# Kernel tuning notes

Hardware: AMD Instinct MI355X
Metric: run time of the kernel (lower is better)

## Reference

```python
import jax, jax.numpy as jnp
import numpy as np
import math

B, S, D, H = 2, 2048, 1024, 16
DK = D // H


def setup_inputs() -> dict:
    key = jax.random.key(0)
    ks = jax.random.split(key, 11)
    s = 1.0 / math.sqrt(D)
    return {
        "q": jax.random.normal(ks[0], (B, S, D), jnp.float32),
        "k": jax.random.normal(ks[1], (B, S, D), jnp.float32),
        "v": jax.random.normal(ks[2], (B, S, D), jnp.float32),
        "Wq": jax.random.normal(ks[3], (D, D), jnp.float32) * s,
        "bq": jnp.zeros((D,), jnp.float32),
        "Wk": jax.random.normal(ks[4], (D, D), jnp.float32) * s,
        "bk": jnp.zeros((D,), jnp.float32),
        "Wv": jax.random.normal(ks[5], (D, D), jnp.float32) * s,
        "bv": jnp.zeros((D,), jnp.float32),
        "Wo": jax.random.normal(ks[6], (D, D), jnp.float32) * s,
        "bo": jnp.zeros((D,), jnp.float32),
        "mask": jnp.ones((B, 1, S), dtype=bool),
    }


def reference(q, k, v, Wq, bq, Wk, bk, Wv, bv, Wo, bo, mask):
    # project and split heads: [B,S,D] -> [B,H,S,DK]
    def proj(x, W, b):
        return (x @ W.T + b).reshape(B, S, H, DK).transpose(0, 2, 1, 3)

    qh, kh, vh = proj(q, Wq, bq), proj(k, Wk, bk), proj(v, Wv, bv)
    scores = jnp.einsum("bhqd,bhkd->bhqk", qh, kh) / math.sqrt(DK)
    # 3D mask [B,1,S], self-attn: expand to [B,1,S,S] via outer AND
    m = mask[:, :, None, :] & mask[:, :, :, None]
    scores = jnp.where(m, scores, -1e9)
    attn = jax.nn.softmax(scores, axis=-1)
    attn = jnp.nan_to_num(attn, nan=0.0, posinf=0.0, neginf=0.0)
    out = jnp.einsum("bhqk,bhkd->bhqd", attn, vh)  # [B,H,S,DK]
    concat = out.transpose(0, 2, 1, 3).reshape(B, S, D)
    return concat @ Wo.T + bo
```

## Files before the change

kernel.cpp:

```cpp
#include <hip/hip_runtime.h>
#include <hip/hip_bf16.h>
#include <stdint.h>

using bf16 = __bf16;
typedef __attribute__((ext_vector_type(8))) __bf16 bf16x8;
typedef __attribute__((ext_vector_type(4))) float f32x4;

typedef const __attribute__((address_space(1))) void* gptr_t;
typedef __attribute__((address_space(3))) void* lptr_t;

__device__ __forceinline__ void gld16(const void* g, void* l) {
    __builtin_amdgcn_global_load_lds((gptr_t)g, (lptr_t)l, 16, 0, 0);
}

__global__ __launch_bounds__(256)
void cvt_kern(const float* __restrict__ in, bf16* __restrict__ out, int n)
{
    const int i = (blockIdx.x * 256 + threadIdx.x) * 8;
    if (i >= n) return;
    const float4 f0 = *(const float4*)(in + i);
    const float4 f1 = *(const float4*)(in + i + 4);
    bf16x8 v = { (bf16)f0.x, (bf16)f0.y, (bf16)f0.z, (bf16)f0.w,
                 (bf16)f1.x, (bf16)f1.y, (bf16)f1.z, (bf16)f1.w };
    *(bf16x8*)(out + i) = v;
}

template<int MODE, bool XWS, bool OUTF32>
__global__ __launch_bounds__(256, 2)
void gemm_mfma(const void* __restrict__ Xv, const bf16* __restrict__ W,
               const float* __restrict__ bias, void* __restrict__ Yv)
{
    constexpr int K = 1024, N = 1024;
    __shared__ bf16 As[64 * 64];
    __shared__ bf16 Bs[128 * 64];

    const int t = threadIdx.x;
    const int w = t >> 6, lane = t & 63, quad = lane >> 4, l15 = lane & 15;
    const int m0 = blockIdx.y * 64, n0 = blockIdx.x * 128;
    const int wm = (w >> 1) * 32, wn = (w & 1) * 64;

    const int srow = t >> 3;
    const int sseg = (t & 7) ^ (srow & 7);

    const float* Xf = (const float*)Xv;
    const bf16*  gA16 = (const bf16*)Xv + (size_t)(m0 + srow) * K + sseg * 8;
    const bf16*  gB   = W + (size_t)(n0 + srow) * K + sseg * 8;

    f32x4 acc[2][4] = {};

    for (int k0 = 0; k0 < K; k0 += 64) {
        if (XWS) {
            gld16(gA16 + k0,          As + t * 8);
            gld16(gA16 + k0 + 32 * K, As + t * 8 + 2048);
        } else {
            #pragma unroll
            for (int r = 0; r < 2; ++r) {
                const int g = r * 256 + t;
                const int row = g >> 3, sg = g & 7;
                const float* p = Xf + (size_t)(m0 + row) * K + k0 + sg * 8;
                const float4 f0 = *(const float4*)p;
                const float4 f1 = *(const float4*)(p + 4);
                bf16x8 vv = { (bf16)f0.x, (bf16)f0.y, (bf16)f0.z, (bf16)f0.w,
                              (bf16)f1.x, (bf16)f1.y, (bf16)f1.z, (bf16)f1.w };
                *(bf16x8*)&As[row * 64 + ((sg ^ (row & 7)) * 8)] = vv;
            }
        }
        gld16(gB + k0,            Bs + t * 8);
        gld16(gB + k0 + 32 * K,   Bs + t * 8 + 2048);
        gld16(gB + k0 + 64 * K,   Bs + t * 8 + 4096);
        gld16(gB + k0 + 96 * K,   Bs + t * 8 + 6144);
        __syncthreads();

        bf16x8 af[2][2], bfr[4][2];
        #pragma unroll
        for (int mt = 0; mt < 2; ++mt)
            #pragma unroll
            for (int kt = 0; kt < 2; ++kt) {
                const int row = wm + mt * 16 + l15;
                const int seg = (kt * 4 + quad) ^ (row & 7);
                af[mt][kt] = *(const bf16x8*)&As[row * 64 + seg * 8];
            }
        #pragma unroll
        for (int nt = 0; nt < 4; ++nt)
            #pragma unroll
            for (int kt = 0; kt < 2; ++kt) {
                const int row = wn + nt * 16 + l15;
                const int seg = (kt * 4 + quad) ^ (row & 7);
                bfr[nt][kt] = *(const bf16x8*)&Bs[row * 64 + seg * 8];
            }
        #pragma unroll
        for (int kt = 0; kt < 2; ++kt)
            #pragma unroll
            for (int mt = 0; mt < 2; ++mt)
                #pragma unroll
                for (int nt = 0; nt < 4; ++nt)
                    acc[mt][nt] = __builtin_amdgcn_mfma_f32_16x16x32_bf16(
                        af[mt][kt], bfr[nt][kt], acc[mt][nt], 0, 0, 0);
        __syncthreads();
    }

    #pragma unroll
    for (int nt = 0; nt < 4; ++nt) {
        const int col = n0 + wn + nt * 16 + l15;
        const float bv = bias[col];
        #pragma unroll
        for (int mt = 0; mt < 2; ++mt)
            #pragma unroll
            for (int i = 0; i < 4; ++i) {
                const int row = m0 + wm + mt * 16 + quad * 4 + i;
                const float v = acc[mt][nt][i] + bv;
                if (MODE == 0) {
                    const size_t off = (size_t)row * N + col;
                    if (OUTF32) ((float*)Yv)[off] = v;
                    else        ((bf16*)Yv)[off]  = (bf16)v;
                } else {
                    const int b = row >> 11, s = row & 2047;
                    const int h = col >> 6, d = col & 63;
                    ((bf16*)Yv)[(((size_t)(b * 16 + h) * 64 + d) << 11) + s] = (bf16)v;
                }
            }
    }
}

__global__ __launch_bounds__(256, 2)
void attn_mfma(const bf16* __restrict__ Q, const bf16* __restrict__ Kg,
               const bf16* __restrict__ Vt, bf16* Cc)
{
    constexpr int S = 2048, D = 1024, DK = 64, LDP = 72;
    __shared__ bf16 Qs[128 * 64];
    __shared__ bf16 Ks[64 * 64];
    __shared__ bf16 Vs[80 * 64];
    __shared__ bf16 Ps[4][32 * LDP];

    const int t = threadIdx.x;
    const int w = t >> 6, lane = t & 63, quad = lane >> 4, l15 = lane & 15;
    const int bh = blockIdx.y, b = bh >> 4, h = bh & 15;
    const int q0 = blockIdx.x * 128;
    const int wq = w * 32;

    const int srow = t >> 3;
    const int sseg = (t & 7) ^ (srow & 7);

    for (int i = t; i < 16 * 64; i += 256) {
        const int r = 64 + (i >> 6);
        Vs[r * 64 + (i & 63)] = (r == 64) ? (bf16)1.0f : (bf16)0.0f;
    }

    {
        const bf16* gQ = Q + (size_t)(b * S + q0 + srow) * D + h * DK + sseg * 8;
        #pragma unroll
        for (int r = 0; r < 4; ++r)
            gld16(gQ + (size_t)(r * 32) * D, Qs + t * 8 + r * 2048);
    }
    __syncthreads();

    bf16x8 aq[2][2];
    #pragma unroll
    for (int mt = 0; mt < 2; ++mt)
        #pragma unroll
        for (int kt = 0; kt < 2; ++kt) {
            const int row = wq + mt * 16 + l15;
            const int seg = (kt * 4 + quad) ^ (row & 7);
            aq[mt][kt] = *(const bf16x8*)&Qs[row * 64 + seg * 8];
        }

    f32x4 o[2][5] = {};
    float mrow[2][4];
    #pragma unroll
    for (int mt = 0; mt < 2; ++mt)
        #pragma unroll
        for (int i = 0; i < 4; ++i) mrow[mt][i] = -1e30f;

    const float c = 0.125f * 1.44269504088896340736f;

    const bf16* gK = Kg + (size_t)(b * S + srow) * D + h * DK + sseg * 8;
    const bf16* gV = Vt + ((size_t)bh * DK + srow) * S + sseg * 8;

    for (int s0 = 0; s0 < S; s0 += 64) {
        gld16(gK + (size_t)s0 * D,        Ks + t * 8);
        gld16(gK + (size_t)(s0 + 32) * D, Ks + t * 8 + 2048);
        gld16(gV + s0,                    Vs + t * 8);
        gld16(gV + s0 + 32 * S,           Vs + t * 8 + 2048);
        __syncthreads();

        f32x4 sa[2][4] = {};
        bf16x8 bk[4][2];
        #pragma unroll
        for (int nt = 0; nt < 4; ++nt)
            #pragma unroll
            for (int kt = 0; kt < 2; ++kt) {
                const int row = nt * 16 + l15;
                const int seg = (kt * 4 + quad) ^ (row & 7);
                bk[nt][kt] = *(const bf16x8*)&Ks[row * 64 + seg * 8];
            }
        #pragma unroll
        for (int kt = 0; kt < 2; ++kt)
            #pragma unroll
            for (int mt = 0; mt < 2; ++mt)
                #pragma unroll
                for (int nt = 0; nt < 4; ++nt)
                    sa[mt][nt] = __builtin_amdgcn_mfma_f32_16x16x32_bf16(
                        aq[mt][kt], bk[nt][kt], sa[mt][nt], 0, 0, 0);

        #pragma unroll
        for (int mt = 0; mt < 2; ++mt)
            #pragma unroll
            for (int i = 0; i < 4; ++i) {
                float v = fmaxf(fmaxf(sa[mt][0][i], sa[mt][1][i]),
                                fmaxf(sa[mt][2][i], sa[mt][3][i])) * c;
                v = fmaxf(v, __shfl_xor(v, 1));
                v = fmaxf(v, __shfl_xor(v, 2));
                v = fmaxf(v, __shfl_xor(v, 4));
                v = fmaxf(v, __shfl_xor(v, 8));
                const float mnew = fmaxf(mrow[mt][i], v);
                const float alpha = __builtin_amdgcn_exp2f(mrow[mt][i] - mnew);
                mrow[mt][i] = mnew;

                const int prow = mt * 16 + quad * 4 + i;
                #pragma unroll
                for (int nt = 0; nt < 4; ++nt) {
                    const float pv = __builtin_amdgcn_exp2f(sa[mt][nt][i] * c - mnew);
                    Ps[w][prow * LDP + nt * 16 + l15] = (bf16)pv;
                }
                #pragma unroll
                for (int nt = 0; nt < 5; ++nt)
                    o[mt][nt][i] *= alpha;
            }

        bf16x8 ap[2][2], bvv[5][2];
        #pragma unroll
        for (int mt = 0; mt < 2; ++mt)
            #pragma unroll
            for (int kt = 0; kt < 2; ++kt) {
                const int row = mt * 16 + l15;
                ap[mt][kt] = *(const bf16x8*)&Ps[w][row * LDP + kt * 32 + quad * 8];
            }
        #pragma unroll
        for (int nt = 0; nt < 5; ++nt)
            #pragma unroll
            for (int kt = 0; kt < 2; ++kt) {
                const int row = nt * 16 + l15;
                const int seg = (kt * 4 + quad) ^ (row & 7);
                bvv[nt][kt] = *(const bf16x8*)&Vs[row * 64 + seg * 8];
            }
        #pragma unroll
        for (int kt = 0; kt < 2; ++kt)
            #pragma unroll
            for (int mt = 0; mt < 2; ++mt)
                #pragma unroll
                for (int nt = 0; nt < 5; ++nt)
                    o[mt][nt] = __builtin_amdgcn_mfma_f32_16x16x32_bf16(
                        ap[mt][kt], bvv[nt][kt], o[mt][nt], 0, 0, 0);

        __syncthreads();
    }

    #pragma unroll
    for (int mt = 0; mt < 2; ++mt)
        #pragma unroll
        for (int i = 0; i < 4; ++i) {
            const int row = q0 + wq + mt * 16 + quad * 4 + i;
            const float lsum = __shfl(o[mt][4][i], quad << 4);
            const float inv = 1.0f / lsum;
            #pragma unroll
            for (int nt = 0; nt < 4; ++nt) {
                const int col = nt * 16 + l15;
                Cc[(size_t)(b * S + row) * D + h * DK + col] = (bf16)(o[mt][nt][i] * inv);
            }
        }
}

extern "C" void kernel_launch(void* const* d_in, const int* in_sizes, int n_in,
                              void* d_out, int out_size, void* d_ws, size_t ws_size,
                              hipStream_t stream)
{
    int iq=0, ik=1, iv=2, iWq=3, ibq=4, iWk=5, ibk=6, iWv=7, ibv=8, iWo=9, ibo=10;
    if (n_in >= 12 && in_sizes[0] == 1048576) {
        iWk=0; iWo=1; iWq=2; iWv=3; ibk=4; ibo=5; ibq=6; ibv=7; ik=8; iq=10; iv=11;
    }

    const float* q  = (const float*)d_in[iq];
    const float* k  = (const float*)d_in[ik];
    const float* v  = (const float*)d_in[iv];
    const float* Wq = (const float*)d_in[iWq];
    const float* bq = (const float*)d_in[ibq];
    const float* Wk = (const float*)d_in[iWk];
    const float* bk = (const float*)d_in[ibk];
    const float* Wv = (const float*)d_in[iWv];
    const float* bv = (const float*)d_in[ibv];
    const float* Wo = (const float*)d_in[iWo];
    const float* bo = (const float*)d_in[ibo];

    bf16* Qp  = (bf16*)d_ws;
    bf16* Kp  = Qp + (size_t)4194304;
    bf16* Vtp = Kp + (size_t)4194304;
    bf16* Wqb = Vtp + (size_t)4194304;
    bf16* Wkb = Wqb + (size_t)1048576;
    bf16* Wvb = Wkb + (size_t)1048576;
    bf16* Wob = Wvb + (size_t)1048576;
    bf16* Cc  = Qp;

    constexpr int WN = 1048576;
    cvt_kern<<<WN / 2048, 256, 0, stream>>>(Wq, Wqb, WN);
    cvt_kern<<<WN / 2048, 256, 0, stream>>>(Wk, Wkb, WN);
    cvt_kern<<<WN / 2048, 256, 0, stream>>>(Wv, Wvb, WN);
    cvt_kern<<<WN / 2048, 256, 0, stream>>>(Wo, Wob, WN);

    dim3 gg(8, 64), bb(256);
    gemm_mfma<0, false, false><<<gg, bb, 0, stream>>>(q, Wqb, bq, Qp);
    gemm_mfma<0, false, false><<<gg, bb, 0, stream>>>(k, Wkb, bk, Kp);
    gemm_mfma<1, false, false><<<gg, bb, 0, stream>>>(v, Wvb, bv, Vtp);
    attn_mfma<<<dim3(16, 32), bb, 0, stream>>>(Qp, Kp, Vtp, Cc);
    gemm_mfma<0, true, true><<<gg, bb, 0, stream>>>(Cc, Wob, bo, d_out);
}
```

Before: 287.8 us.

## Use 8 waves of 16 query rows in attention and skip small max rescales

The attention block grows from 256 to 512 threads: eight waves each own 16 query rows instead of four waves with 32, and each thread now issues one K and one V tile load per iteration instead of two. The online-softmax rescale of the output accumulator is skipped unless some row max grows by more than 8 (in log2 units), which saves exp and multiply work. This trades K/V reuse per wave and register headroom for more waves in flight. The lazy rescale can let unnormalised exponentials reach up to 2^8, which is safe in fp32 but loosens bf16 precision.

```diff
diff --git a/kernel.cpp b/kernel.cpp
--- a/kernel.cpp
+++ b/kernel.cpp
@@ -122,7 +122,7 @@
     }
 }
 
-__global__ __launch_bounds__(256, 2)
+__global__ __launch_bounds__(512, 4)
 void attn_mfma(const bf16* __restrict__ Q, const bf16* __restrict__ Kg,
                const bf16* __restrict__ Vt, bf16* Cc)
 {
@@ -130,46 +130,41 @@
     __shared__ bf16 Qs[128 * 64];
     __shared__ bf16 Ks[64 * 64];
     __shared__ bf16 Vs[80 * 64];
-    __shared__ bf16 Ps[4][32 * LDP];
+    __shared__ bf16 Ps[8][16 * LDP];
 
     const int t = threadIdx.x;
     const int w = t >> 6, lane = t & 63, quad = lane >> 4, l15 = lane & 15;
     const int bh = blockIdx.y, b = bh >> 4, h = bh & 15;
     const int q0 = blockIdx.x * 128;
-    const int wq = w * 32;
+    const int wq = w * 16;
 
     const int srow = t >> 3;
     const int sseg = (t & 7) ^ (srow & 7);
 
-    for (int i = t; i < 16 * 64; i += 256) {
+    for (int i = t; i < 16 * 64; i += 512) {
         const int r = 64 + (i >> 6);
         Vs[r * 64 + (i & 63)] = (r == 64) ? (bf16)1.0f : (bf16)0.0f;
     }
 
     {
         const bf16* gQ = Q + (size_t)(b * S + q0 + srow) * D + h * DK + sseg * 8;
-        #pragma unroll
-        for (int r = 0; r < 4; ++r)
-            gld16(gQ + (size_t)(r * 32) * D, Qs + t * 8 + r * 2048);
+        gld16(gQ,                  Qs + t * 8);
+        gld16(gQ + (size_t)64 * D, Qs + t * 8 + 4096);
     }
     __syncthreads();
 
-    bf16x8 aq[2][2];
-    #pragma unroll
-    for (int mt = 0; mt < 2; ++mt)
-        #pragma unroll
-        for (int kt = 0; kt < 2; ++kt) {
-            const int row = wq + mt * 16 + l15;
-            const int seg = (kt * 4 + quad) ^ (row & 7);
-            aq[mt][kt] = *(const bf16x8*)&Qs[row * 64 + seg * 8];
-        }
-
-    f32x4 o[2][5] = {};
-    float mrow[2][4];
-    #pragma unroll
-    for (int mt = 0; mt < 2; ++mt)
-        #pragma unroll
-        for (int i = 0; i < 4; ++i) mrow[mt][i] = -1e30f;
+    bf16x8 aq[2];
+    #pragma unroll
+    for (int kt = 0; kt < 2; ++kt) {
+        const int row = wq + l15;
+        const int seg = (kt * 4 + quad) ^ (row & 7);
+        aq[kt] = *(const bf16x8*)&Qs[row * 64 + seg * 8];
+    }
+
+    f32x4 o[5] = {};
+    float mrow[4];
+    #pragma unroll
+    for (int i = 0; i < 4; ++i) mrow[i] = -1e30f;
 
     const float c = 0.125f * 1.44269504088896340736f;
 
@@ -177,13 +172,11 @@
     const bf16* gV = Vt + ((size_t)bh * DK + srow) * S + sseg * 8;
 
     for (int s0 = 0; s0 < S; s0 += 64) {
-        gld16(gK + (size_t)s0 * D,        Ks + t * 8);
-        gld16(gK + (size_t)(s0 + 32) * D, Ks + t * 8 + 2048);
-        gld16(gV + s0,                    Vs + t * 8);
-        gld16(gV + s0 + 32 * S,           Vs + t * 8 + 2048);
-        __syncthreads();
-
-        f32x4 sa[2][4] = {};
+        gld16(gK + (size_t)s0 * D, Ks + t * 8);
+        gld16(gV + s0,             Vs + t * 8);
+        __syncthreads();
+
+        f32x4 sa[4] = {};
         bf16x8 bk[4][2];
         #pragma unroll
         for (int nt = 0; nt < 4; ++nt)
@@ -196,45 +189,38 @@
         #pragma unroll
         for (int kt = 0; kt < 2; ++kt)
             #pragma unroll
-            for (int mt = 0; mt < 2; ++mt)
-                #pragma unroll
-                for (int nt = 0; nt < 4; ++nt)
-                    sa[mt][nt] = __builtin_amdgcn_mfma_f32_16x16x32_bf16(
-                        aq[mt][kt], bk[nt][kt], sa[mt][nt], 0, 0, 0);
-
-        #pragma unroll
-        for (int mt = 0; mt < 2; ++mt)
-            #pragma unroll
-            for (int i = 0; i < 4; ++i) {
-                float v = fmaxf(fmaxf(sa[mt][0][i], sa[mt][1][i]),
-                                fmaxf(sa[mt][2][i], sa[mt][3][i])) * c;
-                v = fmaxf(v, __shfl_xor(v, 1));
-                v = fmaxf(v, __shfl_xor(v, 2));
-                v = fmaxf(v, __shfl_xor(v, 4));
-                v = fmaxf(v, __shfl_xor(v, 8));
-                const float mnew = fmaxf(mrow[mt][i], v);
-                const float alpha = __builtin_amdgcn_exp2f(mrow[mt][i] - mnew);
-                mrow[mt][i] = mnew;
-
-                const int prow = mt * 16 + quad * 4 + i;
-                #pragma unroll
-                for (int nt = 0; nt < 4; ++nt) {
-                    const float pv = __builtin_amdgcn_exp2f(sa[mt][nt][i] * c - mnew);
-                    Ps[w][prow * LDP + nt * 16 + l15] = (bf16)pv;
-                }
+            for (int nt = 0; nt < 4; ++nt)
+                sa[nt] = __builtin_amdgcn_mfma_f32_16x16x32_bf16(
+                    aq[kt], bk[nt][kt], sa[nt], 0, 0, 0);
+
+        #pragma unroll
+        for (int i = 0; i < 4; ++i) {
+            float v = fmaxf(fmaxf(sa[0][i], sa[1][i]),
+                            fmaxf(sa[2][i], sa[3][i])) * c;
+            v = fmaxf(v, __shfl_xor(v, 1));
+            v = fmaxf(v, __shfl_xor(v, 2));
+            v = fmaxf(v, __shfl_xor(v, 4));
+            v = fmaxf(v, __shfl_xor(v, 8));
+            if (__any(v > mrow[i] + 8.0f)) {
+                const float mnew = fmaxf(mrow[i], v);
+                const float alpha = __builtin_amdgcn_exp2f(mrow[i] - mnew);
+                mrow[i] = mnew;
                 #pragma unroll
                 for (int nt = 0; nt < 5; ++nt)
-                    o[mt][nt][i] *= alpha;
-            }
-
-        bf16x8 ap[2][2], bvv[5][2];
-        #pragma unroll
-        for (int mt = 0; mt < 2; ++mt)
-            #pragma unroll
-            for (int kt = 0; kt < 2; ++kt) {
-                const int row = mt * 16 + l15;
-                ap[mt][kt] = *(const bf16x8*)&Ps[w][row * LDP + kt * 32 + quad * 8];
-            }
+                    o[nt][i] *= alpha;
+            }
+            const int prow = quad * 4 + i;
+            #pragma unroll
+            for (int nt = 0; nt < 4; ++nt) {
+                const float pv = __builtin_amdgcn_exp2f(sa[nt][i] * c - mrow[i]);
+                Ps[w][prow * LDP + nt * 16 + l15] = (bf16)pv;
+            }
+        }
+
+        bf16x8 ap[2], bvv[5][2];
+        #pragma unroll
+        for (int kt = 0; kt < 2; ++kt)
+            ap[kt] = *(const bf16x8*)&Ps[w][l15 * LDP + kt * 32 + quad * 8];
         #pragma unroll
         for (int nt = 0; nt < 5; ++nt)
             #pragma unroll
@@ -246,28 +232,24 @@
         #pragma unroll
         for (int kt = 0; kt < 2; ++kt)
             #pragma unroll
-            for (int mt = 0; mt < 2; ++mt)
-                #pragma unroll
-                for (int nt = 0; nt < 5; ++nt)
-                    o[mt][nt] = __builtin_amdgcn_mfma_f32_16x16x32_bf16(
-                        ap[mt][kt], bvv[nt][kt], o[mt][nt], 0, 0, 0);
-
-        __syncthreads();
-    }
-
-    #pragma unroll
-    for (int mt = 0; mt < 2; ++mt)
-        #pragma unroll
-        for (int i = 0; i < 4; ++i) {
-            const int row = q0 + wq + mt * 16 + quad * 4 + i;
-            const float lsum = __shfl(o[mt][4][i], quad << 4);
-            const float inv = 1.0f / lsum;
-            #pragma unroll
-            for (int nt = 0; nt < 4; ++nt) {
-                const int col = nt * 16 + l15;
-                Cc[(size_t)(b * S + row) * D + h * DK + col] = (bf16)(o[mt][nt][i] * inv);
-            }
+            for (int nt = 0; nt < 5; ++nt)
+                o[nt] = __builtin_amdgcn_mfma_f32_16x16x32_bf16(
+                    ap[kt], bvv[nt][kt], o[nt], 0, 0, 0);
+
+        __syncthreads();
+    }
+
+    #pragma unroll
+    for (int i = 0; i < 4; ++i) {
+        const int row = q0 + wq + quad * 4 + i;
+        const float lsum = __shfl(o[4][i], quad << 4);
+        const float inv = 1.0f / lsum;
+        #pragma unroll
+        for (int nt = 0; nt < 4; ++nt) {
+            const int col = nt * 16 + l15;
+            Cc[(size_t)(b * S + row) * D + h * DK + col] = (bf16)(o[nt][i] * inv);
         }
+    }
 }
 
 extern "C" void kernel_launch(void* const* d_in, const int* in_sizes, int n_in,
@@ -310,6 +292,6 @@
     gemm_mfma<0, false, false><<<gg, bb, 0, stream>>>(q, Wqb, bq, Qp);
     gemm_mfma<0, false, false><<<gg, bb, 0, stream>>>(k, Wkb, bk, Kp);
     gemm_mfma<1, false, false><<<gg, bb, 0, stream>>>(v, Wvb, bv, Vtp);
-    attn_mfma<<<dim3(16, 32), bb, 0, stream>>>(Qp, Kp, Vtp, Cc);
+    attn_mfma<<<dim3(16, 32), dim3(512), 0, stream>>>(Qp, Kp, Vtp, Cc);
     gemm_mfma<0, true, true><<<gg, bb, 0, stream>>>(Cc, Wob, bo, d_out);
 }
```

Result: faster. 281.1 us (-2.3%).
